# Kernel optimization log

Hardware: AMD Instinct MI355X
Metric: run time of the kernel (lower is better)

The kernel has to match this reference:

```python
import jax, jax.numpy as jnp
import numpy as np

C = 768
TEMB = 512
HID = int(C * 2.0)  # prompt_mlp hidden
K = max(1, int(C * 0.5))  # top-k channels = 384


def silu(x):
    return x * jax.nn.sigmoid(x)


def conv1x1(h, W, b):
    # h: [b,c,H,W], W: [o,c], b: [o]
    return jnp.einsum('bchw,oc->bohw', h, W) + b[None, :, None, None]


def setup_inputs() -> dict:
    key = jax.random.key(0)
    ks = jax.random.split(key, 20)
    s = 0.02
    return {
        'x': jax.random.normal(ks[0], (16, C, 64, 64), jnp.float32),
        'temb': jax.random.normal(ks[1], (16, TEMB), jnp.float32),
        'W_ts': jax.random.normal(ks[2], (2 * C, TEMB), jnp.float32) * s,
        'b_ts': jnp.zeros((2 * C,), jnp.float32),
        'W_tp': jax.random.normal(ks[3], (C, TEMB), jnp.float32) * s,
        'b_tp': jnp.zeros((C,), jnp.float32),
        'W_m1': jax.random.normal(ks[4], (HID, 2 * C), jnp.float32) * s,
        'b_m1': jnp.zeros((HID,), jnp.float32),
        'W_m2': jax.random.normal(ks[5], (C, HID), jnp.float32) * s,
        'b_m2': jnp.zeros((C,), jnp.float32),
        'Wq': jax.random.normal(ks[6], (C, C), jnp.float32) * s,
        'bq': jnp.zeros((C,), jnp.float32),
        'Wk': jax.random.normal(ks[7], (C, C), jnp.float32) * s,
        'bk': jnp.zeros((C,), jnp.float32),
        'Wv': jax.random.normal(ks[8], (C, C), jnp.float32) * s,
        'bv': jnp.zeros((C,), jnp.float32),
        'Wo': jax.random.normal(ks[9], (C, C), jnp.float32) * s,
        'bo': jnp.zeros((C,), jnp.float32),
    }


def reference(x, temb, W_ts, b_ts, W_tp, b_tp, W_m1, b_m1, W_m2, b_m2,
              Wq, bq, Wk, bk, Wv, bv, Wo, bo):
    b, c, H, W = x.shape
    # TimeScaleShift
    ss = silu(temb) @ W_ts.T + b_ts                       # [b, 2c]
    scale, shift = jnp.split(ss, 2, axis=1)
    h = x * (1 + scale[:, :, None, None]) + shift[:, :, None, None]
    # prompt
    gap = h.mean(axis=(2, 3))                             # [b, c]
    tp = silu(temb) @ W_tp.T + b_tp                       # [b, c]
    p = jnp.concatenate([gap, tp], axis=1)                # [b, 2c]
    prompt = silu(p @ W_m1.T + b_m1) @ W_m2.T + b_m2      # [b, c]
    # top-k channel selection
    _, idx = jax.lax.top_k(prompt, K)                     # [b, K]
    bi = jnp.arange(b)[:, None]
    # 1x1 convs then gather selected channels
    q = conv1x1(h, Wq, bq)[bi, idx].reshape(b, K, H * W)
    kf = conv1x1(h, Wk, bk)[bi, idx].reshape(b, K, H * W)
    v = conv1x1(h, Wv, bv)[bi, idx].reshape(b, K, H * W)
    # channel attention
    attn = jax.nn.softmax(jnp.einsum('bkn,bln->bkl', q, kf) * (K ** -0.5), axis=-1)
    out = jnp.einsum('bkl,bln->bkn', attn, v).reshape(b, K, H, W)
    # scatter back into full channel space
    out_full = jnp.zeros_like(h).at[bi, idx].set(out)
    return conv1x1(out_full, Wo, bo)
```

## Files before the change

kernel.cpp:

```cpp
#include <hip/hip_runtime.h>

#define NB 16
#define NC 768
#define NT 512
#define NH 1536
#define KS 384
#define NPX 4096
#define BK 64

typedef __bf16 bfx8 __attribute__((ext_vector_type(8)));
typedef float fx4 __attribute__((ext_vector_type(4)));
typedef unsigned short u16;
typedef unsigned short usv4 __attribute__((ext_vector_type(4)));

__device__ __forceinline__ u16 f2bf(float f) {
  unsigned u = __builtin_bit_cast(unsigned, f);
  u += 0x7FFFu + ((u >> 16) & 1u);
  return (u16)(u >> 16);
}

__device__ __forceinline__ void gload16(const u16* g, u16* l) {
  __builtin_amdgcn_global_load_lds(
      (const __attribute__((address_space(1))) unsigned int*)g,
      (__attribute__((address_space(3))) unsigned int*)l, 16, 0, 0);
}

__global__ void k_trans_mean(const float* __restrict__ x, u16* __restrict__ xT,
                             float* __restrict__ parts) {
  __shared__ float ld[64][65];
  int p0 = blockIdx.x * 64, c0 = blockIdx.y * 64, b = blockIdx.z;
  int t = threadIdx.x;
#pragma unroll
  for (int s = 0; s < 16; ++s) {
    int id = t + 256 * s;
    int i = id >> 6, j = id & 63;
    ld[i][j] = x[(size_t)(b * NC + c0 + i) * NPX + p0 + j];
  }
  __syncthreads();
#pragma unroll
  for (int s = 0; s < 16; ++s) {
    int id = t + 256 * s;
    int j = id >> 6, i = id & 63;
    xT[(size_t)(b * NPX + p0 + j) * NC + c0 + i] = f2bf(ld[i][j]);
  }
  if (t < 64) {
    float s = 0.f;
    for (int j = 0; j < 64; ++j) s += ld[t][j];
    parts[(size_t)(b * NC + c0 + t) * 64 + blockIdx.x] = s;
  }
}

__global__ void k_mean_fin(const float* __restrict__ parts, float* __restrict__ xmean) {
  int id = blockIdx.x * 256 + threadIdx.x;
  if (id >= NB * NC) return;
  float s = 0.f;
  for (int j = 0; j < 64; ++j) s += parts[(size_t)id * 64 + j];
  xmean[id] = s * (1.f / 4096.f);
}

__global__ void k_silu(const float* __restrict__ temb, float* __restrict__ st) {
  int id = blockIdx.x * 256 + threadIdx.x;
  if (id < NB * NT) { float v = temb[id]; st[id] = v / (1.f + expf(-v)); }
}

__global__ void k_mlp8(const float* __restrict__ W, const float* __restrict__ bias,
                       const float* __restrict__ X, float* __restrict__ Y,
                       int len, int nj, int ostride, int obase, int dosilu) {
  __shared__ float Xs[8 * 1537];
  int t = threadIdx.x, lane = t & 63, w = t >> 6;
  int b0 = blockIdx.y * 8;
  int ldx = len + 1;
  for (int id = t; id < 8 * len; id += 256) {
    int bb = id / len, s = id - bb * len;
    Xs[bb * ldx + s] = X[(size_t)(b0 + bb) * len + s];
  }
  __syncthreads();
  for (int i = 0; i < 4; ++i) {
    int j = blockIdx.x * 16 + i * 4 + w;
    if (j < nj) {
      float acc[8] = {0, 0, 0, 0, 0, 0, 0, 0};
      for (int s = lane; s < len; s += 64) {
        float wv = W[(size_t)j * len + s];
#pragma unroll
        for (int bb = 0; bb < 8; ++bb) acc[bb] += wv * Xs[bb * ldx + s];
      }
#pragma unroll
      for (int bb = 0; bb < 8; ++bb) {
        float r = acc[bb];
#pragma unroll
        for (int m = 32; m; m >>= 1) r += __shfl_xor(r, m);
        if (lane == 0) {
          r += bias[j];
          if (dosilu) r = r / (1.f + expf(-r));
          Y[(size_t)(b0 + bb) * ostride + obase + j] = r;
        }
      }
    }
  }
}

__global__ void k_assemble_p(const float* __restrict__ Y1, const float* __restrict__ xmean,
                             float* __restrict__ p) {
  int id = blockIdx.x * 256 + threadIdx.x;
  if (id >= NB * NC) return;
  int b = id / NC, c = id - b * NC;
  const float* yb = Y1 + (size_t)b * 2304;
  p[(size_t)b * 1536 + c] = xmean[id] * (1.f + yb[c]) + yb[768 + c];
  p[(size_t)b * 1536 + 768 + c] = yb[1536 + c];
}

__global__ void k_topk(const float* __restrict__ prompt, int* __restrict__ idx) {
  __shared__ float pr[NC];
  int b = blockIdx.x, t = threadIdx.x;
  for (int c = t; c < NC; c += 256) pr[c] = prompt[(size_t)b * NC + c];
  __syncthreads();
  for (int c = t; c < NC; c += 256) {
    float v = pr[c];
    int r = 0;
    for (int c2 = 0; c2 < NC; ++c2) {
      float v2 = pr[c2];
      r += (v2 > v) || (v2 == v && c2 < c);
    }
    if (r < KS) idx[b * KS + r] = c;
  }
}

__global__ void k_fold(const int* __restrict__ idx, const float* __restrict__ Y1,
                       const float* __restrict__ Wq, const float* __restrict__ bq,
                       const float* __restrict__ Wk, const float* __restrict__ bk,
                       const float* __restrict__ Wv, const float* __restrict__ bv,
                       u16* __restrict__ Aq, float* __restrict__ biasq) {
  __shared__ float red[3 * 256];
  int k = blockIdx.x, b = blockIdx.y, t = threadIdx.x;
  int row = idx[b * KS + k];
  const float* yb = Y1 + (size_t)b * 2304;
  u16* aq = Aq + (size_t)b * 1152 * NC;
  float dq = 0.f, dk = 0.f, dv = 0.f;
  for (int c = t; c < NC; c += 256) {
    float sc = 1.f + yb[c], sh = yb[768 + c];
    float wq = Wq[(size_t)row * NC + c];
    float wk = Wk[(size_t)row * NC + c];
    float wv = Wv[(size_t)row * NC + c];
    aq[(size_t)k * NC + c] = f2bf(wq * sc);
    aq[(size_t)(KS + k) * NC + c] = f2bf(wk * sc);
    aq[(size_t)(2 * KS + k) * NC + c] = f2bf(wv * sc);
    dq += wq * sh; dk += wk * sh; dv += wv * sh;
  }
  red[t] = dq; red[256 + t] = dk; red[512 + t] = dv;
  __syncthreads();
  for (int s = 128; s; s >>= 1) {
    if (t < s) {
      red[t] += red[t + s];
      red[256 + t] += red[256 + t + s];
      red[512 + t] += red[512 + t + s];
    }
    __syncthreads();
  }
  if (t == 0) {
    biasq[b * 1152 + k] = bq[row] + red[0];
    biasq[b * 1152 + KS + k] = bk[row] + red[256];
    biasq[b * 1152 + 2 * KS + k] = bv[row] + red[512];
  }
}

__global__ void k_gather_wo(const int* __restrict__ idx, const float* __restrict__ Wo,
                            u16* __restrict__ WoSel) {
  __shared__ int il[KS];
  int b = blockIdx.y, t = threadIdx.x;
  for (int k = t; k < KS; k += 256) il[k] = idx[b * KS + k];
  __syncthreads();
  int o0 = blockIdx.x * 8;
  for (int oo = 0; oo < 8; ++oo) {
    int o = o0 + oo;
    const float* wr = Wo + (size_t)o * NC;
    u16* dst = WoSel + ((size_t)b * NC + o) * KS;
    for (int k = t; k < KS; k += 256) dst[k] = f2bf(wr[il[k]]);
  }
}

__global__ void k_softmax(const float* __restrict__ Sp, u16* __restrict__ At) {
  __shared__ float sh[2];
  int kk = blockIdx.x, b = blockIdx.y, t = threadIdx.x;
  const size_t stride = (size_t)NB * KS * KS;
  const float* srow = Sp + ((size_t)b * KS + kk) * KS;
  float v[3];
#pragma unroll
  for (int i = 0; i < 3; ++i) {
    int l = t + 128 * i;
    v[i] = srow[l] + srow[stride + l] + srow[2 * stride + l] + srow[3 * stride + l];
  }
  float m = fmaxf(fmaxf(v[0], v[1]), v[2]);
#pragma unroll
  for (int s = 32; s; s >>= 1) m = fmaxf(m, __shfl_xor(m, s));
  if ((t & 63) == 0) sh[t >> 6] = m;
  __syncthreads();
  m = fmaxf(sh[0], sh[1]);
  float e[3];
  float sum = 0.f;
#pragma unroll
  for (int i = 0; i < 3; ++i) { e[i] = expf(v[i] - m); sum += e[i]; }
#pragma unroll
  for (int s = 32; s; s >>= 1) sum += __shfl_xor(sum, s);
  __syncthreads();
  if ((t & 63) == 0) sh[t >> 6] = sum;
  __syncthreads();
  sum = sh[0] + sh[1];
  float inv = 1.f / sum;
#pragma unroll
  for (int i = 0; i < 3; ++i) {
    int l = t + 128 * i;
    At[((size_t)b * KS + l) * KS + kk] = f2bf(e[i] * inv);
  }
}

template <int EPI>
__global__ __launch_bounds__(256, 2) void gemm_bt(
    const u16* __restrict__ A, const u16* __restrict__ Bt, size_t sA, size_t sB,
    int ldA, int ldB, int K, int ksplit, const float* __restrict__ bias,
    float* __restrict__ outF, u16* __restrict__ outU, u16* __restrict__ outU2, float scale) {
  __shared__ u16 As[128 * BK];
  __shared__ u16 Bs[128 * BK];
  int bz = blockIdx.z;
  int b = bz, kbeg = 0, kend = K;
  if (ksplit > 1) {
    b = bz / ksplit;
    int part = bz - b * ksplit;
    int kl = K / ksplit;
    kbeg = part * kl;
    kend = kbeg + kl;
    outF += (size_t)part * NB * KS * KS;
  }
  int m0 = blockIdx.y * 128, n0 = blockIdx.x * 128;
  const u16* Ab = A + (size_t)b * sA;
  const u16* Bb = Bt + (size_t)b * sB;
  int t = threadIdx.x, lane = t & 63, w = t >> 6;
  int wm = (w >> 1) * 64, wn = (w & 1) * 64;
  int r16 = lane & 15, g = lane >> 4;

  int srow = w * 32 + (lane >> 3);
  int scol = (lane & 7) * 8;
  const u16* Ag = Ab + (size_t)(m0 + srow) * ldA + kbeg + scol;
  const u16* Bg = Bb + (size_t)(n0 + srow) * ldB + kbeg + scol;
  u16* Asl = &As[(w * 32) * BK];
  u16* Bsl = &Bs[(w * 32) * BK];

  fx4 acc[4][4] = {};

  for (int k0 = kbeg; k0 < kend; k0 += BK) {
#pragma unroll
    for (int s = 0; s < 4; ++s) gload16(Ag + (size_t)s * 8 * ldA, Asl + s * 8 * BK);
#pragma unroll
    for (int s = 0; s < 4; ++s) gload16(Bg + (size_t)s * 8 * ldB, Bsl + s * 8 * BK);
    Ag += BK; Bg += BK;
    __syncthreads();
#pragma unroll
    for (int kk = 0; kk < 2; ++kk) {
      bfx8 af[4], bfr[4];
#pragma unroll
      for (int i = 0; i < 4; ++i) {
        af[i] = *(const bfx8*)&As[(wm + i * 16 + r16) * BK + kk * 32 + g * 8];
        bfr[i] = *(const bfx8*)&Bs[(wn + i * 16 + r16) * BK + kk * 32 + g * 8];
      }
#pragma unroll
      for (int i = 0; i < 4; ++i)
#pragma unroll
        for (int j = 0; j < 4; ++j)
          acc[i][j] = __builtin_amdgcn_mfma_f32_16x16x32_bf16(af[i], bfr[j], acc[i][j], 0, 0, 0);
    }
    __syncthreads();
  }

#pragma unroll
  for (int i = 0; i < 4; ++i) {
#pragma unroll
    for (int j = 0; j < 4; ++j) {
      int row = m0 + wm + i * 16 + g * 4;
      int col = n0 + wn + j * 16 + r16;
      fx4 v = acc[i][j];
      if constexpr (EPI == 0) {
        const float* bi = bias + b * 1152;
        if (row < 768) {
#pragma unroll
          for (int r = 0; r < 4; ++r)
            outU[((size_t)b * 768 + row + r) * 4096 + col] = f2bf(v[r] + bi[row + r]);
        } else {
          usv4 pk;
#pragma unroll
          for (int r = 0; r < 4; ++r) pk[r] = f2bf(v[r] + bi[row + r]);
          *(usv4*)&outU2[((size_t)b * 4096 + col) * 384 + (row - 768)] = pk;
        }
      } else if constexpr (EPI == 1) {
#pragma unroll
        for (int r = 0; r < 4; ++r)
          outF[((size_t)b * 384 + row + r) * 384 + col] = v[r] * scale;
      } else if constexpr (EPI == 2) {
#pragma unroll
        for (int r = 0; r < 4; ++r)
          outU[((size_t)b * 768 + row + r) * 384 + col] = f2bf(v[r]);
      } else {
#pragma unroll
        for (int r = 0; r < 4; ++r)
          outF[((size_t)b * 768 + row + r) * 4096 + col] = v[r] + bias[row + r];
      }
    }
  }
}

__global__ void k_sentinel(float* out, int n) {
  int id = blockIdx.x * 256 + threadIdx.x;
  if (id < n) out[id] = 12345.0f;
}

extern "C" void kernel_launch(void* const* d_in, const int* in_sizes, int n_in,
                              void* d_out, int out_size, void* d_ws, size_t ws_size,
                              hipStream_t stream) {
  const float* x    = (const float*)d_in[0];
  const float* temb = (const float*)d_in[1];
  const float* W_ts = (const float*)d_in[2];
  const float* b_ts = (const float*)d_in[3];
  const float* W_tp = (const float*)d_in[4];
  const float* b_tp = (const float*)d_in[5];
  const float* W_m1 = (const float*)d_in[6];
  const float* b_m1 = (const float*)d_in[7];
  const float* W_m2 = (const float*)d_in[8];
  const float* b_m2 = (const float*)d_in[9];
  const float* Wq = (const float*)d_in[10];
  const float* bq = (const float*)d_in[11];
  const float* Wk = (const float*)d_in[12];
  const float* bk = (const float*)d_in[13];
  const float* Wv = (const float*)d_in[14];
  const float* bv = (const float*)d_in[15];
  const float* Wo = (const float*)d_in[16];
  const float* bo = (const float*)d_in[17];
  float* out = (float*)d_out;

  char* base = (char*)d_ws;
  size_t off = 0;
  auto alloc = [&](size_t bytes) -> char* {
    char* pp = base + off;
    off += (bytes + 255) & ~(size_t)255;
    return pp;
  };
  u16* xT     = (u16*)alloc((size_t)NB * NPX * NC * 2);
  u16* qk     = (u16*)alloc((size_t)NB * 768 * NPX * 2);
  u16* vT     = (u16*)alloc((size_t)NB * NPX * KS * 2);
  u16* Aq     = (u16*)alloc((size_t)NB * 1152 * NC * 2);
  u16* WoS    = (u16*)alloc((size_t)NB * NC * KS * 2);
  float* parts  = (float*)alloc((size_t)NB * NC * 64 * 4);
  float* xmean  = (float*)alloc((size_t)NB * NC * 4);
  float* Y1     = (float*)alloc((size_t)NB * 2304 * 4);
  float* st     = (float*)alloc((size_t)NB * NT * 4);
  float* p      = (float*)alloc((size_t)NB * 1536 * 4);
  float* hid    = (float*)alloc((size_t)NB * 1536 * 4);
  float* pr     = (float*)alloc((size_t)NB * NC * 4);
  int*   idx    = (int*)alloc((size_t)NB * KS * 4);
  float* biasq  = (float*)alloc((size_t)NB * 1152 * 4);

  if (off > ws_size) {
    k_sentinel<<<(out_size + 255) / 256, 256, 0, stream>>>(out, out_size);
    return;
  }

  float* Sp = (float*)xT;
  u16* At  = (u16*)((char*)xT + 40u * 1024 * 1024);
  u16* Mm  = (u16*)((char*)xT + 48u * 1024 * 1024);

  k_trans_mean<<<dim3(64, 12, NB), 256, 0, stream>>>(x, xT, parts);
  k_mean_fin<<<(NB * NC + 255) / 256, 256, 0, stream>>>(parts, xmean);
  k_silu<<<(NB * NT + 255) / 256, 256, 0, stream>>>(temb, st);
  k_mlp8<<<dim3(96, 2), 256, 0, stream>>>(W_ts, b_ts, st, Y1, 512, 1536, 2304, 0, 0);
  k_mlp8<<<dim3(48, 2), 256, 0, stream>>>(W_tp, b_tp, st, Y1, 512, 768, 2304, 1536, 0);
  k_assemble_p<<<(NB * NC + 255) / 256, 256, 0, stream>>>(Y1, xmean, p);
  k_mlp8<<<dim3(96, 2), 256, 0, stream>>>(W_m1, b_m1, p, hid, 1536, 1536, 1536, 0, 1);
  k_mlp8<<<dim3(48, 2), 256, 0, stream>>>(W_m2, b_m2, hid, pr, 1536, 768, 768, 0, 0);
  k_topk<<<NB, 256, 0, stream>>>(pr, idx);
  k_fold<<<dim3(KS, NB), 256, 0, stream>>>(idx, Y1, Wq, bq, Wk, bk, Wv, bv, Aq, biasq);
  k_gather_wo<<<dim3(96, NB), 256, 0, stream>>>(idx, Wo, WoS);

  gemm_bt<0><<<dim3(32, 9, NB), 256, 0, stream>>>(
      Aq, xT, (size_t)1152 * NC, (size_t)NPX * NC, NC, NC, NC, 1, biasq, nullptr, qk, vT, 0.f);
  gemm_bt<1><<<dim3(3, 3, NB * 4), 256, 0, stream>>>(
      qk, qk + (size_t)KS * NPX, (size_t)768 * NPX, (size_t)768 * NPX, NPX, NPX, NPX, 4,
      nullptr, Sp, nullptr, nullptr, 0.05103103630798287f);
  k_softmax<<<dim3(KS, NB), 128, 0, stream>>>(Sp, At);
  gemm_bt<2><<<dim3(3, 6, NB), 256, 0, stream>>>(
      WoS, At, (size_t)NC * KS, (size_t)KS * KS, KS, KS, KS, 1, nullptr, nullptr, Mm, nullptr, 0.f);
  gemm_bt<3><<<dim3(32, 6, NB), 256, 0, stream>>>(
      Mm, vT, (size_t)NC * KS, (size_t)NPX * KS, KS, KS, KS, 1, bo, out, nullptr, nullptr, 0.f);
}
```

Before: 642.4 us.

## Compute QK scores via per-batch Gram matrix of input instead of Q/K projections

Instead of materializing the selected Q and K projections over all 4096 pixels and then doing a split-K Q·K^T, the code computes the symmetric Gram matrix X·X^T per batch (only the lower-triangular tiles, split into three K-chunks), merges and mirrors it in bf16, then forms S = Aq·(Ak·G)^T. Bias cross-terms are added in the epilogue using the new per-channel sums. This removes the large Q/K intermediate and its 4096-long reduction. The cost is an extra bf16 channel-major copy of x, two extra small GEMMs and a merge pass, plus extra bf16 rounding of G and T, which may affect accuracy. The transpose kernel is also vectorized to float4 loads and packed stores.

```diff
diff --git a/kernel.cpp b/kernel.cpp
--- a/kernel.cpp
+++ b/kernel.cpp
@@ -3,7 +3,6 @@
 #define NB 16
 #define NC 768
 #define NT 512
-#define NH 1536
 #define KS 384
 #define NPX 4096
 #define BK 64
@@ -26,22 +25,27 @@
 }
 
 __global__ void k_trans_mean(const float* __restrict__ x, u16* __restrict__ xT,
-                             float* __restrict__ parts) {
+                             u16* __restrict__ xC, float* __restrict__ parts) {
   __shared__ float ld[64][65];
   int p0 = blockIdx.x * 64, c0 = blockIdx.y * 64, b = blockIdx.z;
   int t = threadIdx.x;
-#pragma unroll
-  for (int s = 0; s < 16; ++s) {
-    int id = t + 256 * s;
-    int i = id >> 6, j = id & 63;
-    ld[i][j] = x[(size_t)(b * NC + c0 + i) * NPX + p0 + j];
-  }
-  __syncthreads();
-#pragma unroll
-  for (int s = 0; s < 16; ++s) {
-    int id = t + 256 * s;
-    int j = id >> 6, i = id & 63;
-    xT[(size_t)(b * NPX + p0 + j) * NC + c0 + i] = f2bf(ld[i][j]);
+  int k = t & 15, ir = t >> 4;
+  int jr = k * 4;
+#pragma unroll
+  for (int s = 0; s < 4; ++s) {
+    int i = ir + s * 16;
+    float4 v = *(const float4*)&x[(size_t)(b * NC + c0 + i) * NPX + p0 + jr];
+    ld[i][jr] = v.x; ld[i][jr + 1] = v.y; ld[i][jr + 2] = v.z; ld[i][jr + 3] = v.w;
+    usv4 pk = {f2bf(v.x), f2bf(v.y), f2bf(v.z), f2bf(v.w)};
+    *(usv4*)&xC[(size_t)(b * NC + c0 + i) * NPX + p0 + jr] = pk;
+  }
+  __syncthreads();
+#pragma unroll
+  for (int s = 0; s < 4; ++s) {
+    int j = ir + s * 16;
+    usv4 pk = {f2bf(ld[k * 4][j]), f2bf(ld[k * 4 + 1][j]),
+               f2bf(ld[k * 4 + 2][j]), f2bf(ld[k * 4 + 3][j])};
+    *(usv4*)&xT[(size_t)(b * NPX + p0 + j) * NC + c0 + k * 4] = pk;
   }
   if (t < 64) {
     float s = 0.f;
@@ -126,18 +130,21 @@
 }
 
 __global__ void k_fold(const int* __restrict__ idx, const float* __restrict__ Y1,
+                       const float* __restrict__ xmean,
                        const float* __restrict__ Wq, const float* __restrict__ bq,
                        const float* __restrict__ Wk, const float* __restrict__ bk,
                        const float* __restrict__ Wv, const float* __restrict__ bv,
-                       u16* __restrict__ Aq, float* __restrict__ biasq) {
-  __shared__ float red[3 * 256];
+                       u16* __restrict__ Aq, float* __restrict__ biasq,
+                       float* __restrict__ sig) {
+  __shared__ float red[5 * 256];
   int k = blockIdx.x, b = blockIdx.y, t = threadIdx.x;
   int row = idx[b * KS + k];
   const float* yb = Y1 + (size_t)b * 2304;
   u16* aq = Aq + (size_t)b * 1152 * NC;
-  float dq = 0.f, dk = 0.f, dv = 0.f;
+  float dq = 0.f, dk = 0.f, dv = 0.f, sq = 0.f, sk = 0.f;
   for (int c = t; c < NC; c += 256) {
     float sc = 1.f + yb[c], sh = yb[768 + c];
+    float xm = xmean[b * NC + c];
     float wq = Wq[(size_t)row * NC + c];
     float wk = Wk[(size_t)row * NC + c];
     float wv = Wv[(size_t)row * NC + c];
@@ -145,14 +152,14 @@
     aq[(size_t)(KS + k) * NC + c] = f2bf(wk * sc);
     aq[(size_t)(2 * KS + k) * NC + c] = f2bf(wv * sc);
     dq += wq * sh; dk += wk * sh; dv += wv * sh;
-  }
-  red[t] = dq; red[256 + t] = dk; red[512 + t] = dv;
+    sq += wq * sc * xm; sk += wk * sc * xm;
+  }
+  red[t] = dq; red[256 + t] = dk; red[512 + t] = dv; red[768 + t] = sq; red[1024 + t] = sk;
   __syncthreads();
   for (int s = 128; s; s >>= 1) {
     if (t < s) {
-      red[t] += red[t + s];
-      red[256 + t] += red[256 + t + s];
-      red[512 + t] += red[512 + t + s];
+#pragma unroll
+      for (int q = 0; q < 5; ++q) red[q * 256 + t] += red[q * 256 + t + s];
     }
     __syncthreads();
   }
@@ -160,6 +167,8 @@
     biasq[b * 1152 + k] = bq[row] + red[0];
     biasq[b * 1152 + KS + k] = bk[row] + red[256];
     biasq[b * 1152 + 2 * KS + k] = bv[row] + red[512];
+    sig[b * NC + k] = 4096.f * red[768];
+    sig[b * NC + KS + k] = 4096.f * red[1024];
   }
 }
 
@@ -178,17 +187,46 @@
   }
 }
 
-__global__ void k_softmax(const float* __restrict__ Sp, u16* __restrict__ At) {
+__global__ void k_gmerge(const float* __restrict__ Gp, u16* __restrict__ G) {
+  __shared__ u16 gl[128][130];
+  int tt = blockIdx.x, b = blockIdx.y, t = threadIdx.x;
+  int i = 0;
+  while ((i + 1) * (i + 2) / 2 <= tt) ++i;
+  int j = tt - i * (i + 1) / 2;
+  const float* p0 = Gp + ((size_t)(0 * NB + b) * 21 + tt) * 16384;
+  const float* p1 = Gp + ((size_t)(1 * NB + b) * 21 + tt) * 16384;
+  const float* p2 = Gp + ((size_t)(2 * NB + b) * 21 + tt) * 16384;
+#pragma unroll
+  for (int s = 0; s < 16; ++s) {
+    int id = t + 256 * s;
+    int row = id >> 5, col4 = (id & 31) * 4;
+    float4 a = *(const float4*)&p0[row * 128 + col4];
+    float4 bb = *(const float4*)&p1[row * 128 + col4];
+    float4 c = *(const float4*)&p2[row * 128 + col4];
+    usv4 pk = {f2bf(a.x + bb.x + c.x), f2bf(a.y + bb.y + c.y),
+               f2bf(a.z + bb.z + c.z), f2bf(a.w + bb.w + c.w)};
+    gl[row][col4] = pk[0]; gl[row][col4 + 1] = pk[1];
+    gl[row][col4 + 2] = pk[2]; gl[row][col4 + 3] = pk[3];
+    *(usv4*)&G[((size_t)b * NC + i * 128 + row) * NC + j * 128 + col4] = pk;
+  }
+  if (i == j) return;
+  __syncthreads();
+#pragma unroll
+  for (int s = 0; s < 16; ++s) {
+    int id = t + 256 * s;
+    int row = id >> 5, col4 = (id & 31) * 4;
+    usv4 pk = {gl[col4][row], gl[col4 + 1][row], gl[col4 + 2][row], gl[col4 + 3][row]};
+    *(usv4*)&G[((size_t)b * NC + j * 128 + row) * NC + i * 128 + col4] = pk;
+  }
+}
+
+__global__ void k_softmax(const float* __restrict__ S, u16* __restrict__ At) {
   __shared__ float sh[2];
   int kk = blockIdx.x, b = blockIdx.y, t = threadIdx.x;
-  const size_t stride = (size_t)NB * KS * KS;
-  const float* srow = Sp + ((size_t)b * KS + kk) * KS;
+  const float* srow = S + ((size_t)b * KS + kk) * KS;
   float v[3];
 #pragma unroll
-  for (int i = 0; i < 3; ++i) {
-    int l = t + 128 * i;
-    v[i] = srow[l] + srow[stride + l] + srow[2 * stride + l] + srow[3 * stride + l];
-  }
+  for (int i = 0; i < 3; ++i) v[i] = srow[t + 128 * i];
   float m = fmaxf(fmaxf(v[0], v[1]), v[2]);
 #pragma unroll
   for (int s = 32; s; s >>= 1) m = fmaxf(m, __shfl_xor(m, s));
@@ -216,21 +254,24 @@
 template <int EPI>
 __global__ __launch_bounds__(256, 2) void gemm_bt(
     const u16* __restrict__ A, const u16* __restrict__ Bt, size_t sA, size_t sB,
-    int ldA, int ldB, int K, int ksplit, const float* __restrict__ bias,
-    float* __restrict__ outF, u16* __restrict__ outU, u16* __restrict__ outU2, float scale) {
+    int ldA, int ldB, int K, const float* __restrict__ bias, int bstride,
+    float* __restrict__ outF, u16* __restrict__ outU, int ldC, size_t sC,
+    const float* __restrict__ sigp, const float* __restrict__ bqp, float scale) {
   __shared__ u16 As[128 * BK];
   __shared__ u16 Bs[128 * BK];
-  int bz = blockIdx.z;
-  int b = bz, kbeg = 0, kend = K;
-  if (ksplit > 1) {
-    b = bz / ksplit;
-    int part = bz - b * ksplit;
-    int kl = K / ksplit;
-    kbeg = part * kl;
-    kend = kbeg + kl;
-    outF += (size_t)part * NB * KS * KS;
-  }
-  int m0 = blockIdx.y * 128, n0 = blockIdx.x * 128;
+  int b, m0, n0, kbeg = 0, kend = K, tt = 0, gpart = 0;
+  if constexpr (EPI == 5) {
+    tt = blockIdx.x;
+    int ii = 0;
+    while ((ii + 1) * (ii + 2) / 2 <= tt) ++ii;
+    int jj = tt - ii * (ii + 1) / 2;
+    m0 = ii * 128; n0 = jj * 128;
+    b = blockIdx.z / 3; gpart = blockIdx.z % 3;
+    kbeg = (gpart == 0) ? 0 : ((gpart == 1) ? 1408 : 2752);
+    kend = (gpart == 0) ? 1408 : ((gpart == 1) ? 2752 : 4096);
+  } else {
+    b = blockIdx.z; m0 = blockIdx.y * 128; n0 = blockIdx.x * 128;
+  }
   const u16* Ab = A + (size_t)b * sA;
   const u16* Bb = Bt + (size_t)b * sB;
   int t = threadIdx.x, lane = t & 63, w = t >> 6;
@@ -274,33 +315,39 @@
   for (int i = 0; i < 4; ++i) {
 #pragma unroll
     for (int j = 0; j < 4; ++j) {
-      int row = m0 + wm + i * 16 + g * 4;
-      int col = n0 + wn + j * 16 + r16;
+      int row = wm + i * 16 + g * 4;
+      int col = wn + j * 16 + r16;
       fx4 v = acc[i][j];
       if constexpr (EPI == 0) {
-        const float* bi = bias + b * 1152;
-        if (row < 768) {
-#pragma unroll
-          for (int r = 0; r < 4; ++r)
-            outU[((size_t)b * 768 + row + r) * 4096 + col] = f2bf(v[r] + bi[row + r]);
-        } else {
-          usv4 pk;
-#pragma unroll
-          for (int r = 0; r < 4; ++r) pk[r] = f2bf(v[r] + bi[row + r]);
-          *(usv4*)&outU2[((size_t)b * 4096 + col) * 384 + (row - 768)] = pk;
+        usv4 pk;
+#pragma unroll
+        for (int r = 0; r < 4; ++r) pk[r] = f2bf(v[r] + bias[b * bstride + m0 + row + r]);
+        *(usv4*)&outU[(size_t)b * sC + (size_t)(n0 + col) * ldC + (m0 + row)] = pk;
+      } else if constexpr (EPI == 1) {
+        int gc = n0 + col;
+        float bk_ = bqp[b * 1152 + 384 + gc];
+        float sk_ = sigp[b * NC + 384 + gc];
+#pragma unroll
+        for (int r = 0; r < 4; ++r) {
+          int gr = m0 + row + r;
+          float bq_ = bqp[b * 1152 + gr];
+          float sq_ = sigp[b * NC + gr];
+          float val = (v[r] + bq_ * sk_ + bk_ * sq_ + 4096.f * bq_ * bk_) * scale;
+          outF[(size_t)b * sC + (size_t)gr * ldC + gc] = val;
         }
-      } else if constexpr (EPI == 1) {
+      } else if constexpr (EPI == 2) {
 #pragma unroll
         for (int r = 0; r < 4; ++r)
-          outF[((size_t)b * 384 + row + r) * 384 + col] = v[r] * scale;
-      } else if constexpr (EPI == 2) {
+          outU[(size_t)b * sC + (size_t)(m0 + row + r) * ldC + (n0 + col)] = f2bf(v[r]);
+      } else if constexpr (EPI == 3) {
 #pragma unroll
         for (int r = 0; r < 4; ++r)
-          outU[((size_t)b * 768 + row + r) * 384 + col] = f2bf(v[r]);
+          outF[(size_t)b * sC + (size_t)(m0 + row + r) * ldC + (n0 + col)] =
+              v[r] + bias[b * bstride + m0 + row + r];
       } else {
-#pragma unroll
-        for (int r = 0; r < 4; ++r)
-          outF[((size_t)b * 768 + row + r) * 4096 + col] = v[r] + bias[row + r];
+        float* o = outF + ((size_t)(gpart * NB + b) * 21 + tt) * 16384;
+#pragma unroll
+        for (int r = 0; r < 4; ++r) o[(row + r) * 128 + col] = v[r];
       }
     }
   }
@@ -341,11 +388,11 @@
     off += (bytes + 255) & ~(size_t)255;
     return pp;
   };
-  u16* xT     = (u16*)alloc((size_t)NB * NPX * NC * 2);
-  u16* qk     = (u16*)alloc((size_t)NB * 768 * NPX * 2);
-  u16* vT     = (u16*)alloc((size_t)NB * NPX * KS * 2);
-  u16* Aq     = (u16*)alloc((size_t)NB * 1152 * NC * 2);
-  u16* WoS    = (u16*)alloc((size_t)NB * NC * KS * 2);
+  u16* xT   = (u16*)alloc((size_t)NB * NPX * NC * 2);
+  u16* xC   = (u16*)alloc((size_t)NB * NC * NPX * 2);
+  u16* vT   = (u16*)alloc((size_t)NB * NPX * KS * 2);
+  u16* Aq   = (u16*)alloc((size_t)NB * 1152 * NC * 2);
+  u16* WoS  = (u16*)alloc((size_t)NB * NC * KS * 2);
   float* parts  = (float*)alloc((size_t)NB * NC * 64 * 4);
   float* xmean  = (float*)alloc((size_t)NB * NC * 4);
   float* Y1     = (float*)alloc((size_t)NB * 2304 * 4);
@@ -355,17 +402,21 @@
   float* pr     = (float*)alloc((size_t)NB * NC * 4);
   int*   idx    = (int*)alloc((size_t)NB * KS * 4);
   float* biasq  = (float*)alloc((size_t)NB * 1152 * 4);
+  float* sig    = (float*)alloc((size_t)NB * NC * 4);
 
   if (off > ws_size) {
     k_sentinel<<<(out_size + 255) / 256, 256, 0, stream>>>(out, out_size);
     return;
   }
 
-  float* Sp = (float*)xT;
-  u16* At  = (u16*)((char*)xT + 40u * 1024 * 1024);
-  u16* Mm  = (u16*)((char*)xT + 48u * 1024 * 1024);
-
-  k_trans_mean<<<dim3(64, 12, NB), 256, 0, stream>>>(x, xT, parts);
+  float* Gp = (float*)xT;
+  u16* G  = (u16*)xC;
+  u16* T  = (u16*)((char*)xC + 20u * 1024 * 1024);
+  float* S = (float*)((char*)xC + 30u * 1024 * 1024);
+  u16* At = (u16*)((char*)xC + 40u * 1024 * 1024);
+  u16* Mm = (u16*)((char*)xC + 46u * 1024 * 1024);
+
+  k_trans_mean<<<dim3(64, 12, NB), 256, 0, stream>>>(x, xT, xC, parts);
   k_mean_fin<<<(NB * NC + 255) / 256, 256, 0, stream>>>(parts, xmean);
   k_silu<<<(NB * NT + 255) / 256, 256, 0, stream>>>(temb, st);
   k_mlp8<<<dim3(96, 2), 256, 0, stream>>>(W_ts, b_ts, st, Y1, 512, 1536, 2304, 0, 0);
@@ -374,17 +425,27 @@
   k_mlp8<<<dim3(96, 2), 256, 0, stream>>>(W_m1, b_m1, p, hid, 1536, 1536, 1536, 0, 1);
   k_mlp8<<<dim3(48, 2), 256, 0, stream>>>(W_m2, b_m2, hid, pr, 1536, 768, 768, 0, 0);
   k_topk<<<NB, 256, 0, stream>>>(pr, idx);
-  k_fold<<<dim3(KS, NB), 256, 0, stream>>>(idx, Y1, Wq, bq, Wk, bk, Wv, bv, Aq, biasq);
+  k_fold<<<dim3(KS, NB), 256, 0, stream>>>(idx, Y1, xmean, Wq, bq, Wk, bk, Wv, bv, Aq, biasq, sig);
   k_gather_wo<<<dim3(96, NB), 256, 0, stream>>>(idx, Wo, WoS);
 
-  gemm_bt<0><<<dim3(32, 9, NB), 256, 0, stream>>>(
-      Aq, xT, (size_t)1152 * NC, (size_t)NPX * NC, NC, NC, NC, 1, biasq, nullptr, qk, vT, 0.f);
-  gemm_bt<1><<<dim3(3, 3, NB * 4), 256, 0, stream>>>(
-      qk, qk + (size_t)KS * NPX, (size_t)768 * NPX, (size_t)768 * NPX, NPX, NPX, NPX, 4,
-      nullptr, Sp, nullptr, nullptr, 0.05103103630798287f);
-  k_softmax<<<dim3(KS, NB), 128, 0, stream>>>(Sp, At);
+  gemm_bt<0><<<dim3(32, 3, NB), 256, 0, stream>>>(
+      Aq + (size_t)2 * KS * NC, xT, (size_t)1152 * NC, (size_t)NPX * NC, NC, NC, NC,
+      biasq + 2 * KS, 1152, nullptr, vT, KS, (size_t)NPX * KS, nullptr, nullptr, 0.f);
+  gemm_bt<5><<<dim3(21, 1, NB * 3), 256, 0, stream>>>(
+      xC, xC, (size_t)NC * NPX, (size_t)NC * NPX, NPX, NPX, NPX,
+      nullptr, 0, Gp, nullptr, 0, 0, nullptr, nullptr, 0.f);
+  k_gmerge<<<dim3(21, NB), 256, 0, stream>>>(Gp, G);
+  gemm_bt<2><<<dim3(6, 3, NB), 256, 0, stream>>>(
+      Aq + (size_t)KS * NC, G, (size_t)1152 * NC, (size_t)NC * NC, NC, NC, NC,
+      nullptr, 0, nullptr, T, NC, (size_t)KS * NC, nullptr, nullptr, 0.f);
+  gemm_bt<1><<<dim3(3, 3, NB), 256, 0, stream>>>(
+      Aq, T, (size_t)1152 * NC, (size_t)KS * NC, NC, NC, NC,
+      nullptr, 0, S, nullptr, KS, (size_t)KS * KS, sig, biasq, 0.05103103630798287f);
+  k_softmax<<<dim3(KS, NB), 128, 0, stream>>>(S, At);
   gemm_bt<2><<<dim3(3, 6, NB), 256, 0, stream>>>(
-      WoS, At, (size_t)NC * KS, (size_t)KS * KS, KS, KS, KS, 1, nullptr, nullptr, Mm, nullptr, 0.f);
+      WoS, At, (size_t)NC * KS, (size_t)KS * KS, KS, KS, KS,
+      nullptr, 0, nullptr, Mm, KS, (size_t)NC * KS, nullptr, nullptr, 0.f);
   gemm_bt<3><<<dim3(32, 6, NB), 256, 0, stream>>>(
-      Mm, vT, (size_t)NC * KS, (size_t)NPX * KS, KS, KS, KS, 1, bo, out, nullptr, nullptr, 0.f);
-}
+      Mm, vT, (size_t)NC * KS, (size_t)NPX * KS, KS, KS, KS,
+      bo, 0, out, nullptr, NPX, (size_t)NC * NPX, nullptr, nullptr, 0.f);
+}
```

New measurement: 675.4 us. 1.05x slower.
